# Kernel tuning notes

Hardware: AMD Instinct MI355X
Metric: run time of the kernel (lower is better)

Reference implementation:

```python
import jax, jax.numpy as jnp
import numpy as np

DIM = 64; HEADS = 8; WIN = 4; K = 3
B = 8; H = 256; W = 256; WS = H // 2  # 2x2 window grid since ka_win_num=4
L = WIN * K * K            # 36 tokens for kernel self-attention
DH = DIM // HEADS
RED = DIM // 16            # SE reduction (dim>=64 branch)


def setup_inputs() -> dict:
    key = jax.random.key(0)
    ks = jax.random.split(key, 12)
    f = lambda k, s: jax.random.normal(k, s, jnp.float32) * 0.05
    return {
        "x": jax.random.normal(ks[0], (B, DIM, H, W), jnp.float32),
        "conv_w": f(ks[1], (WIN, DIM, DIM, K, K)),   # per-window Conv2d weights
        "w_qkv": f(ks[2], (3 * DIM, DIM)),
        "b_qkv": f(ks[3], (3 * DIM,)),
        "w_out": f(ks[4], (DIM, DIM)),
        "b_out": f(ks[5], (DIM,)),
        "se_w1": f(ks[6], (WIN, RED, DIM)),
        "se_b1": f(ks[7], (WIN, RED)),
        "se_w2": f(ks[8], (WIN, DIM, RED)),
        "se_b2": f(ks[9], (WIN, DIM)),
        "ln_w": jnp.ones((DIM,), jnp.float32),
        "ln_b": jnp.zeros((DIM,), jnp.float32),
    }


def reference(x, conv_w, w_qkv, b_qkv, w_out, b_out,
              se_w1, se_b1, se_w2, se_b2, ln_w, ln_b):
    Bx, C, Hx, Wx = x.shape
    ws = WS
    xw = x.reshape(Bx, C, 2, ws, 2, ws).transpose(2, 4, 0, 1, 3, 5)
    xw = xw.reshape(WIN, Bx, C, ws, ws)

    # ---- kernels from conv weights (conv output itself is discarded upstream)
    kern = conv_w.reshape(WIN, DIM, DIM, K * K).transpose(1, 0, 3, 2).reshape(DIM, L, DIM)

    # ---- tiny multi-head self-attention over the L kernel tokens, batch = DIM
    qkv = kern @ w_qkv.T + b_qkv                       # (DIM, L, 3*DIM)
    qkv = qkv.reshape(DIM, L, 3, HEADS, DH).transpose(2, 0, 3, 1, 4)  # (3, DIM, H, L, DH)
    q = qkv[0] * (DH ** -0.5)
    k_, v = qkv[1], qkv[2]
    attn = jax.nn.softmax(jnp.einsum('bhld,bhmd->bhlm', q, k_), axis=-1)
    out = jnp.einsum('bhlm,bhmd->bhld', attn, v)        # (DIM, H, L, DH)
    out = out.transpose(0, 2, 1, 3).reshape(DIM, L, DIM)
    kern = out @ w_out.T + b_out                        # (DIM, L, DIM)
    kern = kern.reshape(DIM, WIN, K, K, DIM).transpose(1, 0, 4, 2, 3)

    # ---- SE gating per window: pool over spatial, two 1x1 convs, sigmoid gate
    pooled = kern.mean(axis=(3, 4))
    h = jax.nn.relu(jnp.einsum('woi,wri->wor', pooled, se_w1) + se_b1[:, None, :])
    s = jax.nn.sigmoid(jnp.einsum('wor,wir->woi', h, se_w2) + se_b2[:, None, :])
    kern = kern * s[:, :, :, None, None]

    # ---- dynamic per-window conv2d (stride 1, pad 1)
    conv = lambda xi, wi: jax.lax.conv_general_dilated(
        xi, wi, window_strides=(1, 1), padding=((1, 1), (1, 1)))
    yw = jax.vmap(conv)(xw, kern)

    # ---- window reverse -> (B, C, H, W)
    y = yw.reshape(2, 2, Bx, C, ws, ws).transpose(2, 3, 0, 4, 1, 5).reshape(Bx, C, Hx, Wx)

    # ---- channel-last LayerNorm, then residual
    yt = y.transpose(0, 2, 3, 1)
    mu = yt.mean(-1, keepdims=True)
    var = yt.var(-1, keepdims=True)
    yt = (yt - mu) / jnp.sqrt(var + 1e-5) * ln_w + ln_b
    return x + yt.transpose(0, 3, 1, 2)
```

## Files before the change

kernel.cpp:

```cpp
#include <hip/hip_runtime.h>
#include <hip/hip_fp16.h>


typedef __attribute__((ext_vector_type(8))) _Float16 half8;
typedef __attribute__((ext_vector_type(4))) float floatx4;
typedef unsigned short ushort_t;

__device__ __forceinline__ ushort_t f2h(float f) {
  union { _Float16 h; ushort_t u; } cv;
  cv.h = (_Float16)f;
  return cv.u;
}

__device__ __align__(16) ushort_t g_W2[4 * 9 * 64 * 64];

__global__ __launch_bounds__(256) void tw_kernel(
    const float* __restrict__ conv_w,
    const float* __restrict__ w_qkv,
    const float* __restrict__ b_qkv,
    const float* __restrict__ w_out,
    const float* __restrict__ b_out,
    const float* __restrict__ se_w1,
    const float* __restrict__ se_b1,
    const float* __restrict__ se_w2,
    const float* __restrict__ se_b2)
{
  __shared__ __align__(16) float smem[11952];
  const int t = threadIdx.x;
  const int o = blockIdx.x;
  float* k0   = smem;
  float* qkvb = smem + 2448;
  float* aout = smem + 9504;

  for (int idx = t; idx < 36 * 64; idx += 256) {
    int l = idx >> 6, i = idx & 63;
    int win = l / 9, t9 = l - win * 9;
    k0[l * 68 + i] = conv_w[((win * 64 + o) * 64 + i) * 9 + t9];
  }
  __syncthreads();

  for (int idx = t; idx < 48 * 36; idx += 256) {
    int jg = idx / 36, l = idx - jg * 36;
    int j = jg << 2;
    const float* kr = k0 + l * 68;
    const float* w0 = w_qkv + j * 64;
    float a0 = 0.f, a1 = 0.f, a2 = 0.f, a3 = 0.f;
    #pragma unroll
    for (int i = 0; i < 64; i += 4) {
      floatx4 kf  = *(const floatx4*)(kr + i);
      floatx4 wf0 = *(const floatx4*)(w0 + i);
      floatx4 wf1 = *(const floatx4*)(w0 + 64 + i);
      floatx4 wf2 = *(const floatx4*)(w0 + 128 + i);
      floatx4 wf3 = *(const floatx4*)(w0 + 192 + i);
      #pragma unroll
      for (int e = 0; e < 4; ++e) {
        a0 += kf[e] * wf0[e];
        a1 += kf[e] * wf1[e];
        a2 += kf[e] * wf2[e];
        a3 += kf[e] * wf3[e];
      }
    }
    floatx4 r = { a0 + b_qkv[j],     a1 + b_qkv[j + 1],
                  a2 + b_qkv[j + 2], a3 + b_qkv[j + 3] };
    *(floatx4*)(qkvb + l * 196 + j) = r;
  }
  __syncthreads();

  for (int idx = t; idx < 288; idx += 256) {
    int h = idx / 36, l = idx - h * 36;
    const int hq = h << 3;
    floatx4 q0 = *(const floatx4*)(qkvb + l * 196 + hq);
    floatx4 q1 = *(const floatx4*)(qkvb + l * 196 + hq + 4);
    float sc[36];
    float mx = -1e30f;
    #pragma unroll
    for (int m = 0; m < 36; ++m) {
      const float* kr = qkvb + m * 196 + 64 + hq;
      floatx4 k0f = *(const floatx4*)(kr);
      floatx4 k1f = *(const floatx4*)(kr + 4);
      float s = 0.f;
      #pragma unroll
      for (int e = 0; e < 4; ++e) s += q0[e] * k0f[e];
      #pragma unroll
      for (int e = 0; e < 4; ++e) s += q1[e] * k1f[e];
      s *= 0.35355339059327373f;
      sc[m] = s;
      mx = fmaxf(mx, s);
    }
    float den = 0.f;
    #pragma unroll
    for (int m = 0; m < 36; ++m) { sc[m] = __expf(sc[m] - mx); den += sc[m]; }
    float a[8];
    #pragma unroll
    for (int e = 0; e < 8; ++e) a[e] = 0.f;
    #pragma unroll
    for (int m = 0; m < 36; ++m) {
      const float* vr = qkvb + m * 196 + 128 + hq;
      floatx4 v0f = *(const floatx4*)(vr);
      floatx4 v1f = *(const floatx4*)(vr + 4);
      float p = sc[m];
      #pragma unroll
      for (int e = 0; e < 4; ++e) { a[e] += p * v0f[e]; a[e + 4] += p * v1f[e]; }
    }
    float inv = 1.f / den;
    floatx4 o0, o1;
    #pragma unroll
    for (int e = 0; e < 4; ++e) { o0[e] = a[e] * inv; o1[e] = a[e + 4] * inv; }
    *(floatx4*)(aout + l * 68 + hq) = o0;
    *(floatx4*)(aout + l * 68 + hq + 4) = o1;
  }
  __syncthreads();

  float* mat = k0;
  for (int idx = t; idx < 16 * 36; idx += 256) {
    int og = idx / 36, l = idx - og * 36;
    int oo = og << 2;
    const float* ar = aout + l * 68;
    const float* w0 = w_out + oo * 64;
    float a0 = 0.f, a1 = 0.f, a2 = 0.f, a3 = 0.f;
    #pragma unroll
    for (int i = 0; i < 64; i += 4) {
      floatx4 af  = *(const floatx4*)(ar + i);
      floatx4 wf0 = *(const floatx4*)(w0 + i);
      floatx4 wf1 = *(const floatx4*)(w0 + 64 + i);
      floatx4 wf2 = *(const floatx4*)(w0 + 128 + i);
      floatx4 wf3 = *(const floatx4*)(w0 + 192 + i);
      #pragma unroll
      for (int e = 0; e < 4; ++e) {
        a0 += af[e] * wf0[e];
        a1 += af[e] * wf1[e];
        a2 += af[e] * wf2[e];
        a3 += af[e] * wf3[e];
      }
    }
    floatx4 r = { a0 + b_out[oo],     a1 + b_out[oo + 1],
                  a2 + b_out[oo + 2], a3 + b_out[oo + 3] };
    *(floatx4*)(mat + l * 68 + oo) = r;
  }
  __syncthreads();

  float* pl = qkvb;
  float* h1 = qkvb + 256;
  {
    int win = t >> 6, I = t & 63;
    float p = 0.f;
    #pragma unroll
    for (int t9 = 0; t9 < 9; ++t9) p += mat[(win * 9 + t9) * 68 + I];
    pl[t] = p * (1.f / 9.f);
  }
  __syncthreads();
  if (t < 16) {
    int win = t >> 2, r = t & 3;
    const float* wr = se_w1 + (win * 4 + r) * 64;
    const float* pr = pl + (win << 6);
    float a = se_b1[win * 4 + r];
    #pragma unroll 8
    for (int i = 0; i < 64; ++i) a += pr[i] * wr[i];
    h1[t] = fmaxf(a, 0.f);
  }
  __syncthreads();
  {
    int win = t >> 6, I = t & 63;
    float a = se_b2[(win << 6) + I];
    #pragma unroll
    for (int r = 0; r < 4; ++r)
      a += h1[win * 4 + r] * se_w2[((win << 6) + I) * 4 + r];
    float s = 1.f / (1.f + __expf(-a));
    #pragma unroll
    for (int t9 = 0; t9 < 9; ++t9) {
      float v = mat[(win * 9 + t9) * 68 + I] * s;
      g_W2[((win * 9 + t9) * 64 + o) * 64 + I] = f2h(v);
    }
  }
}

__global__ __launch_bounds__(256, 3) void conv_kernel(
    const float* __restrict__ x,
    const float* __restrict__ ln_w,
    const float* __restrict__ ln_b,
    float* __restrict__ outp)
{
  __shared__ __align__(16) short xs[24480];
  int* xs32 = (int*)xs;
  const int t = threadIdx.x;
  const int wb = blockIdx.x & 7;
  const int hb = (blockIdx.x >> 3) & 31;
  const int b  = blockIdx.x >> 8;
  const int gh0 = hb << 3, gw0 = wb << 5;
  const int hlo = (gh0 >= 128) ? 128 : 0;
  const int wlo = (gw0 >= 128) ? 128 : 0;
  const int win = ((gh0 >= 128) ? 2 : 0) + ((gw0 >= 128) ? 1 : 0);
  const float* xb = x + ((size_t)b << 22);

  #pragma unroll
  for (int it = 0; it < 5; ++it) {
    int idx = t + it * 256;
    int u = idx & 3;
    int r = (idx >> 2) % 10;
    int cp = idx / 40;
    int gh = gh0 + r - 1;
    int gw = gw0 + (u << 3);
    floatx4 a0 = {0.f, 0.f, 0.f, 0.f}, a1 = a0, b0 = a0, b1 = a0;
    if (gh >= hlo && gh < hlo + 128) {
      const float* p = xb + ((size_t)(2 * cp) << 16) + gh * 256 + gw;
      a0 = *(const floatx4*)p;
      a1 = *(const floatx4*)(p + 4);
      b0 = *(const floatx4*)(p + 65536);
      b1 = *(const floatx4*)(p + 65540);
    }
    int base = (r * 34 + (u << 3) + 1) * 36 + cp;
    #pragma unroll
    for (int j = 0; j < 4; ++j) {
      unsigned int pv = (unsigned int)f2h(a0[j]) |
                        ((unsigned int)f2h(b0[j]) << 16);
      xs32[base + j * 36] = (int)pv;
    }
    #pragma unroll
    for (int j = 0; j < 4; ++j) {
      unsigned int pv = (unsigned int)f2h(a1[j]) |
                        ((unsigned int)f2h(b1[j]) << 16);
      xs32[base + (j + 4) * 36] = (int)pv;
    }
  }
  #pragma unroll
  for (int it = 0; it < 3; ++it) {
    int idx = t + it * 256;
    if (idx < 640) {
      int e = idx & 1;
      int r = (idx >> 1) % 10;
      int cp = idx / 20;
      int gh = gh0 + r - 1;
      int gw = e ? (gw0 + 32) : (gw0 - 1);
      int cl = e ? 33 : 0;
      unsigned int pv = 0;
      if (gh >= hlo && gh < hlo + 128 && gw >= wlo && gw < wlo + 128) {
        const float* p = xb + ((size_t)(2 * cp) << 16) + gh * 256 + gw;
        pv = (unsigned int)f2h(p[0]) | ((unsigned int)f2h(p[65536]) << 16);
      }
      xs32[(r * 34 + cl) * 36 + cp] = (int)pv;
    }
  }
  __syncthreads();

  const int wave = t >> 6, lane = t & 63;
  const int l15 = lane & 15, q = lane >> 4;

  floatx4 acc[4][4];
  #pragma unroll
  for (int mt = 0; mt < 4; ++mt)
    #pragma unroll
    for (int nt = 0; nt < 4; ++nt)
      acc[mt][nt] = (floatx4){0.f, 0.f, 0.f, 0.f};

  int aoff[4];
  #pragma unroll
  for (int mt = 0; mt < 4; ++mt)
    aoff[mt] = ((2 * wave + (mt >> 1)) * 34 + ((mt & 1) << 4) + l15) * 72 + (q << 3);

  const ushort_t* Wb = g_W2 + win * 36864 + l15 * 64 + (q << 3);
  half8 bcur[4], bnxt[4];
  #pragma unroll
  for (int nt = 0; nt < 4; ++nt)
    bcur[nt] = *(const half8*)(Wb + nt * 1024);

  #pragma unroll
  for (int tap = 0; tap < 9; ++tap) {
    const int ky = tap / 3, kx = tap - ky * 3;
    const int toff = (ky * 34 + kx) * 72;
    #pragma unroll
    for (int kc = 0; kc < 2; ++kc) {
      const int nit = tap * 2 + kc + 1;
      if (nit < 18) {
        const int ntap = nit >> 1, nkc = nit & 1;
        #pragma unroll
        for (int nt = 0; nt < 4; ++nt)
          bnxt[nt] = *(const half8*)(Wb + ntap * 4096 + nkc * 32 + nt * 1024);
      }
      half8 av[4];
      #pragma unroll
      for (int mt = 0; mt < 4; ++mt)
        av[mt] = *(const half8*)(xs + aoff[mt] + toff + kc * 32);
      #pragma unroll
      for (int mt = 0; mt < 4; ++mt)
        #pragma unroll
        for (int nt = 0; nt < 4; ++nt)
          acc[mt][nt] = __builtin_amdgcn_mfma_f32_16x16x32_f16(
              av[mt], bcur[nt], acc[mt][nt], 0, 0, 0);
      #pragma unroll
      for (int nt = 0; nt < 4; ++nt) bcur[nt] = bnxt[nt];
    }
  }

  float lnwv[4], lnbv[4];
  #pragma unroll
  for (int nt = 0; nt < 4; ++nt) {
    int c = (nt << 4) + l15;
    lnwv[nt] = ln_w[c];
    lnbv[nt] = ln_b[c];
  }
  #pragma unroll
  for (int mt = 0; mt < 4; ++mt) {
    const int rr = 2 * wave + (mt >> 1);
    const int colb = (mt & 1) << 4;
    float s1[4], s2[4];
    #pragma unroll
    for (int e = 0; e < 4; ++e) { s1[e] = 0.f; s2[e] = 0.f; }
    #pragma unroll
    for (int nt = 0; nt < 4; ++nt)
      #pragma unroll
      for (int e = 0; e < 4; ++e) {
        float v = acc[mt][nt][e];
        s1[e] += v;
        s2[e] += v * v;
      }
    #pragma unroll
    for (int m = 1; m < 16; m <<= 1) {
      #pragma unroll
      for (int e = 0; e < 4; ++e) {
        s1[e] += __shfl_xor(s1[e], m, 64);
        s2[e] += __shfl_xor(s2[e], m, 64);
      }
    }
    float mean[4], rstd[4];
    #pragma unroll
    for (int e = 0; e < 4; ++e) {
      mean[e] = s1[e] * 0.015625f;
      float var = s2[e] * 0.015625f - mean[e] * mean[e];
      rstd[e] = rsqrtf(var + 1e-5f);
    }
    #pragma unroll
    for (int nt = 0; nt < 4; ++nt) {
      const int c = (nt << 4) + l15;
      const size_t goff = ((size_t)(b * 64 + c) << 16) +
                          (gh0 + rr) * 256 + gw0 + colb + (q << 2);
      floatx4 xr = *(const floatx4*)(x + goff);
      floatx4 v;
      #pragma unroll
      for (int e = 0; e < 4; ++e)
        v[e] = (acc[mt][nt][e] - mean[e]) * rstd[e] * lnwv[nt] + lnbv[nt] + xr[e];
      *(floatx4*)(outp + goff) = v;
    }
  }
}

extern "C" void kernel_launch(void* const* d_in, const int* in_sizes, int n_in,
                              void* d_out, int out_size, void* d_ws, size_t ws_size,
                              hipStream_t stream) {
  const float* x     = (const float*)d_in[0];
  const float* convw = (const float*)d_in[1];
  const float* wqkv  = (const float*)d_in[2];
  const float* bqkv  = (const float*)d_in[3];
  const float* wout  = (const float*)d_in[4];
  const float* bout  = (const float*)d_in[5];
  const float* sew1  = (const float*)d_in[6];
  const float* seb1  = (const float*)d_in[7];
  const float* sew2  = (const float*)d_in[8];
  const float* seb2  = (const float*)d_in[9];
  const float* lnw   = (const float*)d_in[10];
  const float* lnb   = (const float*)d_in[11];
  float* outp = (float*)d_out;

  hipLaunchKernelGGL(tw_kernel, dim3(64), dim3(256), 0, stream,
                     convw, wqkv, bqkv, wout, bout,
                     sew1, seb1, sew2, seb2);
  hipLaunchKernelGGL(conv_kernel, dim3(2048), dim3(256), 0, stream,
                     x, lnw, lnb, outp);
}
```

Measured before the change: 400.8 us.

## Make conv blocks persistent over four column chunks with register-prefetched input tiles

```diff
diff --git a/kernel.cpp b/kernel.cpp
--- a/kernel.cpp
+++ b/kernel.cpp
@@ -174,7 +174,7 @@
   }
 }
 
-__global__ __launch_bounds__(256, 3) void conv_kernel(
+__global__ __launch_bounds__(256, 2) void conv_kernel(
     const float* __restrict__ x,
     const float* __restrict__ ln_w,
     const float* __restrict__ ln_b,
@@ -183,74 +183,90 @@
   __shared__ __align__(16) short xs[24480];
   int* xs32 = (int*)xs;
   const int t = threadIdx.x;
-  const int wb = blockIdx.x & 7;
-  const int hb = (blockIdx.x >> 3) & 31;
-  const int b  = blockIdx.x >> 8;
-  const int gh0 = hb << 3, gw0 = wb << 5;
+  const int wsb = blockIdx.x & 1;
+  const int hb  = (blockIdx.x >> 1) & 31;
+  const int b   = blockIdx.x >> 6;
+  const int gh0 = hb << 3;
+  const int gws = wsb << 7;
   const int hlo = (gh0 >= 128) ? 128 : 0;
-  const int wlo = (gw0 >= 128) ? 128 : 0;
-  const int win = ((gh0 >= 128) ? 2 : 0) + ((gw0 >= 128) ? 1 : 0);
+  const int wlo = gws;
+  const int win = ((gh0 >= 128) ? 2 : 0) + wsb;
   const float* xb = x + ((size_t)b << 22);
 
-  #pragma unroll
-  for (int it = 0; it < 5; ++it) {
-    int idx = t + it * 256;
-    int u = idx & 3;
-    int r = (idx >> 2) % 10;
-    int cp = idx / 40;
-    int gh = gh0 + r - 1;
-    int gw = gw0 + (u << 3);
-    floatx4 a0 = {0.f, 0.f, 0.f, 0.f}, a1 = a0, b0 = a0, b1 = a0;
-    if (gh >= hlo && gh < hlo + 128) {
-      const float* p = xb + ((size_t)(2 * cp) << 16) + gh * 256 + gw;
-      a0 = *(const floatx4*)p;
-      a1 = *(const floatx4*)(p + 4);
-      b0 = *(const floatx4*)(p + 65536);
-      b1 = *(const floatx4*)(p + 65540);
-    }
-    int base = (r * 34 + (u << 3) + 1) * 36 + cp;
-    #pragma unroll
-    for (int j = 0; j < 4; ++j) {
-      unsigned int pv = (unsigned int)f2h(a0[j]) |
-                        ((unsigned int)f2h(b0[j]) << 16);
-      xs32[base + j * 36] = (int)pv;
-    }
-    #pragma unroll
-    for (int j = 0; j < 4; ++j) {
-      unsigned int pv = (unsigned int)f2h(a1[j]) |
-                        ((unsigned int)f2h(b1[j]) << 16);
-      xs32[base + (j + 4) * 36] = (int)pv;
-    }
-  }
-  #pragma unroll
-  for (int it = 0; it < 3; ++it) {
-    int idx = t + it * 256;
-    if (idx < 640) {
-      int e = idx & 1;
-      int r = (idx >> 1) % 10;
-      int cp = idx / 20;
+  floatx4 sa0[5], sa1[5], sb0[5], sb1[5];
+  float se0[3], se1[3];
+
+  auto load_regs = [&](int gw0) {
+    #pragma unroll
+    for (int it = 0; it < 5; ++it) {
+      int idx = t + it * 256;
+      int u = idx & 3;
+      int r = (idx >> 2) % 10;
+      int cp = idx / 40;
       int gh = gh0 + r - 1;
-      int gw = e ? (gw0 + 32) : (gw0 - 1);
-      int cl = e ? 33 : 0;
-      unsigned int pv = 0;
-      if (gh >= hlo && gh < hlo + 128 && gw >= wlo && gw < wlo + 128) {
+      int gw = gw0 + (u << 3);
+      floatx4 z = {0.f, 0.f, 0.f, 0.f};
+      sa0[it] = z; sa1[it] = z; sb0[it] = z; sb1[it] = z;
+      if (gh >= hlo && gh < hlo + 128) {
         const float* p = xb + ((size_t)(2 * cp) << 16) + gh * 256 + gw;
-        pv = (unsigned int)f2h(p[0]) | ((unsigned int)f2h(p[65536]) << 16);
-      }
-      xs32[(r * 34 + cl) * 36 + cp] = (int)pv;
-    }
-  }
-  __syncthreads();
+        sa0[it] = *(const floatx4*)p;
+        sa1[it] = *(const floatx4*)(p + 4);
+        sb0[it] = *(const floatx4*)(p + 65536);
+        sb1[it] = *(const floatx4*)(p + 65540);
+      }
+    }
+    #pragma unroll
+    for (int it = 0; it < 3; ++it) {
+      int idx = t + it * 256;
+      se0[it] = 0.f; se1[it] = 0.f;
+      if (idx < 640) {
+        int e = idx & 1;
+        int r = (idx >> 1) % 10;
+        int cp = idx / 20;
+        int gh = gh0 + r - 1;
+        int gw = e ? (gw0 + 32) : (gw0 - 1);
+        if (gh >= hlo && gh < hlo + 128 && gw >= wlo && gw < wlo + 128) {
+          const float* p = xb + ((size_t)(2 * cp) << 16) + gh * 256 + gw;
+          se0[it] = p[0];
+          se1[it] = p[65536];
+        }
+      }
+    }
+  };
+
+  auto write_lds = [&]() {
+    #pragma unroll
+    for (int it = 0; it < 5; ++it) {
+      int idx = t + it * 256;
+      int u = idx & 3;
+      int r = (idx >> 2) % 10;
+      int cp = idx / 40;
+      int base = (r * 34 + (u << 3) + 1) * 36 + cp;
+      #pragma unroll
+      for (int j = 0; j < 4; ++j)
+        xs32[base + j * 36] = (int)((unsigned)f2h(sa0[it][j]) |
+                                    ((unsigned)f2h(sb0[it][j]) << 16));
+      #pragma unroll
+      for (int j = 0; j < 4; ++j)
+        xs32[base + (j + 4) * 36] = (int)((unsigned)f2h(sa1[it][j]) |
+                                          ((unsigned)f2h(sb1[it][j]) << 16));
+    }
+    #pragma unroll
+    for (int it = 0; it < 3; ++it) {
+      int idx = t + it * 256;
+      if (idx < 640) {
+        int e = idx & 1;
+        int r = (idx >> 1) % 10;
+        int cp = idx / 20;
+        int cl = e ? 33 : 0;
+        xs32[(r * 34 + cl) * 36 + cp] = (int)((unsigned)f2h(se0[it]) |
+                                              ((unsigned)f2h(se1[it]) << 16));
+      }
+    }
+  };
 
   const int wave = t >> 6, lane = t & 63;
   const int l15 = lane & 15, q = lane >> 4;
-
-  floatx4 acc[4][4];
-  #pragma unroll
-  for (int mt = 0; mt < 4; ++mt)
-    #pragma unroll
-    for (int nt = 0; nt < 4; ++nt)
-      acc[mt][nt] = (floatx4){0.f, 0.f, 0.f, 0.f};
 
   int aoff[4];
   #pragma unroll
@@ -258,38 +274,6 @@
     aoff[mt] = ((2 * wave + (mt >> 1)) * 34 + ((mt & 1) << 4) + l15) * 72 + (q << 3);
 
   const ushort_t* Wb = g_W2 + win * 36864 + l15 * 64 + (q << 3);
-  half8 bcur[4], bnxt[4];
-  #pragma unroll
-  for (int nt = 0; nt < 4; ++nt)
-    bcur[nt] = *(const half8*)(Wb + nt * 1024);
-
-  #pragma unroll
-  for (int tap = 0; tap < 9; ++tap) {
-    const int ky = tap / 3, kx = tap - ky * 3;
-    const int toff = (ky * 34 + kx) * 72;
-    #pragma unroll
-    for (int kc = 0; kc < 2; ++kc) {
-      const int nit = tap * 2 + kc + 1;
-      if (nit < 18) {
-        const int ntap = nit >> 1, nkc = nit & 1;
-        #pragma unroll
-        for (int nt = 0; nt < 4; ++nt)
-          bnxt[nt] = *(const half8*)(Wb + ntap * 4096 + nkc * 32 + nt * 1024);
-      }
-      half8 av[4];
-      #pragma unroll
-      for (int mt = 0; mt < 4; ++mt)
-        av[mt] = *(const half8*)(xs + aoff[mt] + toff + kc * 32);
-      #pragma unroll
-      for (int mt = 0; mt < 4; ++mt)
-        #pragma unroll
-        for (int nt = 0; nt < 4; ++nt)
-          acc[mt][nt] = __builtin_amdgcn_mfma_f32_16x16x32_f16(
-              av[mt], bcur[nt], acc[mt][nt], 0, 0, 0);
-      #pragma unroll
-      for (int nt = 0; nt < 4; ++nt) bcur[nt] = bnxt[nt];
-    }
-  }
 
   float lnwv[4], lnbv[4];
   #pragma unroll
@@ -298,47 +282,109 @@
     lnwv[nt] = ln_w[c];
     lnbv[nt] = ln_b[c];
   }
-  #pragma unroll
-  for (int mt = 0; mt < 4; ++mt) {
-    const int rr = 2 * wave + (mt >> 1);
-    const int colb = (mt & 1) << 4;
-    float s1[4], s2[4];
-    #pragma unroll
-    for (int e = 0; e < 4; ++e) { s1[e] = 0.f; s2[e] = 0.f; }
+
+  load_regs(gws);
+  write_lds();
+  __syncthreads();
+
+  #pragma unroll 1
+  for (int c = 0; c < 4; ++c) {
+    const int gw0 = gws + (c << 5);
+    if (c < 3) load_regs(gws + ((c + 1) << 5));
+
+    floatx4 acc[4][4];
+    #pragma unroll
+    for (int mt = 0; mt < 4; ++mt)
+      #pragma unroll
+      for (int nt = 0; nt < 4; ++nt)
+        acc[mt][nt] = (floatx4){0.f, 0.f, 0.f, 0.f};
+
+    half8 bcur[4], bnxt[4];
     #pragma unroll
     for (int nt = 0; nt < 4; ++nt)
+      bcur[nt] = *(const half8*)(Wb + nt * 1024);
+
+    #pragma unroll
+    for (int tap = 0; tap < 9; ++tap) {
+      const int ky = tap / 3, kx = tap - ky * 3;
+      const int toff = (ky * 34 + kx) * 72;
+      #pragma unroll
+      for (int kc = 0; kc < 2; ++kc) {
+        const int nit = tap * 2 + kc + 1;
+        if (nit < 18) {
+          const int ntap = nit >> 1, nkc = nit & 1;
+          #pragma unroll
+          for (int nt = 0; nt < 4; ++nt)
+            bnxt[nt] = *(const half8*)(Wb + ntap * 4096 + nkc * 32 + nt * 1024);
+        }
+        half8 av[4];
+        #pragma unroll
+        for (int mt = 0; mt < 4; ++mt)
+          av[mt] = *(const half8*)(xs + aoff[mt] + toff + kc * 32);
+        #pragma unroll
+        for (int mt = 0; mt < 4; ++mt)
+          #pragma unroll
+          for (int nt = 0; nt < 4; ++nt)
+            acc[mt][nt] = __builtin_amdgcn_mfma_f32_16x16x32_f16(
+                av[mt], bcur[nt], acc[mt][nt], 0, 0, 0);
+        #pragma unroll
+        for (int nt = 0; nt < 4; ++nt) bcur[nt] = bnxt[nt];
+      }
+    }
+
+    #pragma unroll
+    for (int mt = 0; mt < 4; ++mt) {
+      const int rr = 2 * wave + (mt >> 1);
+      const int colb = (mt & 1) << 4;
+      floatx4 xr[4];
+      size_t goffs[4];
+      #pragma unroll
+      for (int nt = 0; nt < 4; ++nt) {
+        const int ch = (nt << 4) + l15;
+        goffs[nt] = ((size_t)(b * 64 + ch) << 16) +
+                    (gh0 + rr) * 256 + gw0 + colb + (q << 2);
+        xr[nt] = *(const floatx4*)(x + goffs[nt]);
+      }
+      float s1[4], s2[4];
+      #pragma unroll
+      for (int e = 0; e < 4; ++e) { s1[e] = 0.f; s2[e] = 0.f; }
+      #pragma unroll
+      for (int nt = 0; nt < 4; ++nt)
+        #pragma unroll
+        for (int e = 0; e < 4; ++e) {
+          float v = acc[mt][nt][e];
+          s1[e] += v;
+          s2[e] += v * v;
+        }
+      #pragma unroll
+      for (int m = 1; m < 16; m <<= 1) {
+        #pragma unroll
+        for (int e = 0; e < 4; ++e) {
+          s1[e] += __shfl_xor(s1[e], m, 64);
+          s2[e] += __shfl_xor(s2[e], m, 64);
+        }
+      }
+      float mean[4], rstd[4];
       #pragma unroll
       for (int e = 0; e < 4; ++e) {
-        float v = acc[mt][nt][e];
-        s1[e] += v;
-        s2[e] += v * v;
-      }
-    #pragma unroll
-    for (int m = 1; m < 16; m <<= 1) {
-      #pragma unroll
-      for (int e = 0; e < 4; ++e) {
-        s1[e] += __shfl_xor(s1[e], m, 64);
-        s2[e] += __shfl_xor(s2[e], m, 64);
-      }
-    }
-    float mean[4], rstd[4];
-    #pragma unroll
-    for (int e = 0; e < 4; ++e) {
-      mean[e] = s1[e] * 0.015625f;
-      float var = s2[e] * 0.015625f - mean[e] * mean[e];
-      rstd[e] = rsqrtf(var + 1e-5f);
-    }
-    #pragma unroll
-    for (int nt = 0; nt < 4; ++nt) {
-      const int c = (nt << 4) + l15;
-      const size_t goff = ((size_t)(b * 64 + c) << 16) +
-                          (gh0 + rr) * 256 + gw0 + colb + (q << 2);
-      floatx4 xr = *(const floatx4*)(x + goff);
-      floatx4 v;
-      #pragma unroll
-      for (int e = 0; e < 4; ++e)
-        v[e] = (acc[mt][nt][e] - mean[e]) * rstd[e] * lnwv[nt] + lnbv[nt] + xr[e];
-      *(floatx4*)(outp + goff) = v;
+        mean[e] = s1[e] * 0.015625f;
+        float var = s2[e] * 0.015625f - mean[e] * mean[e];
+        rstd[e] = rsqrtf(var + 1e-5f);
+      }
+      #pragma unroll
+      for (int nt = 0; nt < 4; ++nt) {
+        floatx4 v;
+        #pragma unroll
+        for (int e = 0; e < 4; ++e)
+          v[e] = (acc[mt][nt][e] - mean[e]) * rstd[e] * lnwv[nt] + lnbv[nt] + xr[nt][e];
+        *(floatx4*)(outp + goffs[nt]) = v;
+      }
+    }
+
+    if (c < 3) {
+      __syncthreads();
+      write_lds();
+      __syncthreads();
     }
   }
 }
@@ -363,6 +409,6 @@
   hipLaunchKernelGGL(tw_kernel, dim3(64), dim3(256), 0, stream,
                      convw, wqkv, bqkv, wout, bout,
                      sew1, seb1, sew2, seb2);
-  hipLaunchKernelGGL(conv_kernel, dim3(2048), dim3(256), 0, stream,
+  hipLaunchKernelGGL(conv_kernel, dim3(512), dim3(256), 0, stream,
                      x, lnw, lnb, outp);
 }
```

Result: slower. 495.8 us (+23.7%).
